# Kernel optimization log

Hardware: AMD Instinct MI355X
Metric: run time of the kernel (lower is better)

Reference implementation:

```python
import jax, jax.numpy as jnp
import numpy as np

N_NODES = 20000  # number of batch nodes (static for segment ops)

def setup_inputs() -> dict:
    key = jax.random.key(0)
    N, E, V, D = N_NODES, 640000, 100000, 64
    ks = jax.random.split(key, 8)
    nodes = jax.random.randint(ks[0], (N,), 0, V)
    neigh_idx = jax.random.randint(ks[1], (E,), 0, V)
    seg_ids = jnp.sort(jax.random.randint(ks[2], (E,), 0, N))  # ragged degrees, sorted by node
    u2e = jax.random.normal(ks[3], (V, D), jnp.float32) * 0.02
    s1 = 1.0 / np.sqrt(2 * D)
    s2 = 1.0 / np.sqrt(D)
    att1_w = jax.random.uniform(ks[4], (2 * D, D), jnp.float32, -s1, s1)
    att1_b = jnp.zeros((D,), jnp.float32)
    att2_w = jax.random.uniform(ks[5], (D, D), jnp.float32, -s2, s2)
    att2_b = jnp.zeros((D,), jnp.float32)
    att3_w = jax.random.uniform(ks[6], (D, 1), jnp.float32, -s2, s2)
    att3_b = jnp.zeros((1,), jnp.float32)
    return dict(nodes=nodes, neigh_idx=neigh_idx, seg_ids=seg_ids, u2e=u2e,
                att1_w=att1_w, att1_b=att1_b, att2_w=att2_w, att2_b=att2_b,
                att3_w=att3_w, att3_b=att3_b)


def reference(nodes, neigh_idx, seg_ids, u2e, att1_w, att1_b, att2_w, att2_b, att3_w, att3_b):
    # Ragged per-node neighbor attention, flattened over all edges.
    e_u = u2e[neigh_idx]              # [E, D] neighbor embeddings
    u_rep = u2e[nodes][seg_ids]       # [E, D] center-node embedding broadcast per edge
    x = jnp.concatenate([e_u, u_rep], axis=1)            # [E, 2D]
    x = jax.nn.relu(x @ att1_w + att1_b)                  # [E, D]
    x = jax.nn.relu(x @ att2_w + att2_b)                  # [E, D]
    logits = (x @ att3_w + att3_b)[:, 0]                  # [E]
    # segment softmax over each node's neighbor set
    m = jax.ops.segment_max(logits, seg_ids, num_segments=N_NODES)
    m = jnp.where(jnp.isfinite(m), m, 0.0)                # guard empty segments
    ex = jnp.exp(logits - m[seg_ids])
    denom = jax.ops.segment_sum(ex, seg_ids, num_segments=N_NODES)
    att = ex / jnp.maximum(denom[seg_ids], 1e-9)          # [E]
    # attention-weighted sum of neighbor embeddings per node (e_u^T @ att_w per node)
    out = jax.ops.segment_sum(att[:, None] * e_u, seg_ids, num_segments=N_NODES)  # [N, D]
    return out
```

## Files before the change

### kernel.cpp

```cpp
#include <hip/hip_runtime.h>
#include <hip/hip_bf16.h>

typedef __attribute__((ext_vector_type(8))) short bf16x8;
typedef __attribute__((ext_vector_type(4))) float f32x4;

__device__ __forceinline__ unsigned short f2bf(float f) {
    unsigned x = __float_as_uint(f);
    unsigned r = (x + 0x7FFF + ((x >> 16) & 1)) >> 16;
    return (unsigned short)r;
}
__device__ __forceinline__ bf16x8 cvt8(const float* __restrict__ p) {
    bf16x8 r;
#pragma unroll
    for (int j = 0; j < 8; ++j) r[j] = (short)f2bf(p[j]);
    return r;
}
__device__ __forceinline__ unsigned pack_relu_bf16(unsigned yv, unsigned zv) {
    float lo = fmaxf(__uint_as_float(yv << 16) + __uint_as_float(zv << 16), 0.0f);
    float hi = fmaxf(__uint_as_float(yv & 0xFFFF0000u) + __uint_as_float(zv & 0xFFFF0000u), 0.0f);
    __hip_bfloat162 p = __float22bfloat162_rn(float2{lo, hi});
    return *(unsigned*)&p;
}

__global__ void prep_bounds_k(const float* __restrict__ w1,
                              const float* __restrict__ w2,
                              const int* __restrict__ segs,
                              unsigned short* __restrict__ w1t,
                              unsigned short* __restrict__ w2t,
                              int* __restrict__ seg_off, int N, int E) {
    int t = threadIdx.x;
    if (blockIdx.x == 0) {
        for (int i = t; i < 128 * 64; i += 256) {
            int k = i >> 6, n = i & 63;
            w1t[n * 128 + k] = f2bf(w1[i]);
        }
        for (int i = t; i < 64 * 64; i += 256) {
            int k = i >> 6, n = i & 63;
            w2t[n * 64 + k] = f2bf(w2[i]);
        }
    } else {
        int idx = (blockIdx.x - 1) * 256 + t;
        if (idx > N) return;
        int l = 0, r = E;
        while (l < r) { int mid = (l + r) >> 1; if (segs[mid] < idx) l = mid + 1; else r = mid; }
        seg_off[idx] = l;
    }
}

template <bool BF>
__launch_bounds__(256)
__global__ void conv_y_z_k(const float* __restrict__ u2e,
                           const int* __restrict__ nodes,
                           const unsigned short* __restrict__ w1t,
                           const float* __restrict__ b1f,
                           unsigned short* __restrict__ u2ebf,
                           unsigned short* __restrict__ Y,
                           unsigned short* __restrict__ z,
                           int V, int N, int yblocks) {
    const int wid = threadIdx.x >> 6;
    const int lane = threadIdx.x & 63;
    const int q = lane >> 4;
    const int m15 = lane & 15;

    if ((int)blockIdx.x < yblocks) {
        const int wbase = (blockIdx.x * 4 + wid) * 16;
        if (wbase >= V) return;
        int row = min(wbase + m15, V - 1);
        const float* p = u2e + (long)row * 64;
        bf16x8 a0 = cvt8(p + q * 8);
        bf16x8 a1 = cvt8(p + 32 + q * 8);
        if (BF && wbase + m15 < V) {
            *(bf16x8*)(u2ebf + (long)row * 64 + q * 8) = a0;
            *(bf16x8*)(u2ebf + (long)row * 64 + 32 + q * 8) = a1;
        }
        f32x4 acc[4];
#pragma unroll
        for (int b = 0; b < 4; ++b) {
            acc[b] = (f32x4){0.f, 0.f, 0.f, 0.f};
            const bf16x8* wrow = (const bf16x8*)(w1t + (b * 16 + m15) * 128);
            acc[b] = __builtin_amdgcn_mfma_f32_16x16x32_bf16(a0, wrow[0 + q], acc[b], 0, 0, 0);
            acc[b] = __builtin_amdgcn_mfma_f32_16x16x32_bf16(a1, wrow[4 + q], acc[b], 0, 0, 0);
        }
#pragma unroll
        for (int b = 0; b < 4; ++b)
#pragma unroll
            for (int r = 0; r < 4; ++r) {
                int rr = wbase + q * 4 + r;
                if (rr < V) Y[(long)rr * 64 + b * 16 + m15] = f2bf(acc[b][r]);
            }
    } else {
        const int wbase = (((int)blockIdx.x - yblocks) * 4 + wid) * 16;
        if (wbase >= N) return;
        int nd = nodes[min(wbase + m15, N - 1)];
        const float* p = u2e + (long)nd * 64;
        bf16x8 a0 = cvt8(p + q * 8);
        bf16x8 a1 = cvt8(p + 32 + q * 8);
        f32x4 acc[4];
#pragma unroll
        for (int b = 0; b < 4; ++b) {
            float bv = b1f[b * 16 + m15];
            acc[b] = (f32x4){bv, bv, bv, bv};
            const bf16x8* wrow = (const bf16x8*)(w1t + (b * 16 + m15) * 128);
            acc[b] = __builtin_amdgcn_mfma_f32_16x16x32_bf16(a0, wrow[8 + q], acc[b], 0, 0, 0);
            acc[b] = __builtin_amdgcn_mfma_f32_16x16x32_bf16(a1, wrow[12 + q], acc[b], 0, 0, 0);
        }
#pragma unroll
        for (int b = 0; b < 4; ++b)
#pragma unroll
            for (int r = 0; r < 4; ++r) {
                int rr = wbase + q * 4 + r;
                if (rr < N) z[(long)rr * 64 + b * 16 + m15] = f2bf(acc[b][r]);
            }
    }
}

__launch_bounds__(256)
__global__ void logits2_k(const int* __restrict__ neigh,
                          const int* __restrict__ segs,
                          const unsigned short* __restrict__ Y,
                          const unsigned short* __restrict__ z,
                          const unsigned short* __restrict__ w2t,
                          const float* __restrict__ b2f,
                          const float* __restrict__ w3f, const float* __restrict__ b3f,
                          float* __restrict__ ex, int E) {
    const int wid = threadIdx.x >> 6;
    const int lane = threadIdx.x & 63;
    const int q = lane >> 4;
    const int m15 = lane & 15;
    const long base = ((long)blockIdx.x * 4 + wid) * 32;
    if (base >= E) return;

    int vi[2], sg[2];
#pragma unroll
    for (int g = 0; g < 2; ++g) {
        long e = base + g * 16 + m15;
        int ec = (int)(e < E ? e : (long)E - 1);
        vi[g] = neigh[ec];
        sg[g] = segs[ec];
    }
    bf16x8 y0[2], y1[2], zz0[2], zz1[2];
#pragma unroll
    for (int g = 0; g < 2; ++g) {
        const unsigned short* yr = Y + (long)vi[g] * 64;
        y0[g] = *(const bf16x8*)(yr + q * 8);
        y1[g] = *(const bf16x8*)(yr + 32 + q * 8);
        const unsigned short* zr = z + (long)sg[g] * 64;
        zz0[g] = *(const bf16x8*)(zr + q * 8);
        zz1[g] = *(const bf16x8*)(zr + 32 + q * 8);
    }

    f32x4 acc[2][4];
#pragma unroll
    for (int g = 0; g < 2; ++g) {
        bf16x8 h0, h1;
#pragma unroll
        for (int j = 0; j < 4; ++j) {
            ((unsigned*)&h0)[j] = pack_relu_bf16(((unsigned*)&y0[g])[j], ((unsigned*)&zz0[g])[j]);
            ((unsigned*)&h1)[j] = pack_relu_bf16(((unsigned*)&y1[g])[j], ((unsigned*)&zz1[g])[j]);
        }
#pragma unroll
        for (int b = 0; b < 4; ++b) {
            float bv = b2f[b * 16 + m15];
            acc[g][b] = (f32x4){bv, bv, bv, bv};
            const bf16x8* wrow = (const bf16x8*)(w2t + (b * 16 + m15) * 64);
            acc[g][b] = __builtin_amdgcn_mfma_f32_16x16x32_bf16(h0, wrow[0 + q], acc[g][b], 0, 0, 0);
            acc[g][b] = __builtin_amdgcn_mfma_f32_16x16x32_bf16(h1, wrow[4 + q], acc[g][b], 0, 0, 0);
        }
    }

    const float b3v = b3f[0];
#pragma unroll
    for (int g = 0; g < 2; ++g)
#pragma unroll
        for (int r = 0; r < 4; ++r) {
            float v = 0.0f;
#pragma unroll
            for (int b = 0; b < 4; ++b) v += fmaxf(acc[g][b][r], 0.0f) * w3f[b * 16 + m15];
            v += __shfl_xor(v, 1);
            v += __shfl_xor(v, 2);
            v += __shfl_xor(v, 4);
            v += __shfl_xor(v, 8);
            long ee = base + g * 16 + q * 4 + r;
            if (m15 == r && ee < E) ex[ee] = __expf(v + b3v);
        }
}

template <bool BF>
__launch_bounds__(256)
__global__ void aggw_k(const int* __restrict__ seg_off,
                       const int* __restrict__ neigh,
                       const unsigned short* __restrict__ u2ebf,
                       const float* __restrict__ u2e,
                       const float* __restrict__ ex,
                       float* __restrict__ out, int N) {
    const int wid = threadIdx.x >> 6;
    const int lane = threadIdx.x & 63;
    const int n = blockIdx.x * 4 + wid;
    if (n >= N) return;
    const int lo = seg_off[n];
    const int hi = seg_off[n + 1];
    const int slot = lane >> 3;
    const int cl = lane & 7;

    float a[8] = {0.f, 0.f, 0.f, 0.f, 0.f, 0.f, 0.f, 0.f};
    float s = 0.0f;

    for (int e = lo + slot; e < hi; e += 8) {
        float w = ex[e];
        int vi = neigh[e];
        s += w;
        if constexpr (BF) {
            bf16x8 v = *(const bf16x8*)(u2ebf + (long)vi * 64 + cl * 8);
            const unsigned* vd = (const unsigned*)&v;
#pragma unroll
            for (int j = 0; j < 4; ++j) {
                a[2 * j]     = fmaf(w, __uint_as_float(vd[j] << 16), a[2 * j]);
                a[2 * j + 1] = fmaf(w, __uint_as_float(vd[j] & 0xFFFF0000u), a[2 * j + 1]);
            }
        } else {
            const float* row = u2e + (long)vi * 64 + cl * 8;
            float4 v0 = *(const float4*)row;
            float4 v1 = *(const float4*)(row + 4);
            a[0] = fmaf(w, v0.x, a[0]); a[1] = fmaf(w, v0.y, a[1]);
            a[2] = fmaf(w, v0.z, a[2]); a[3] = fmaf(w, v0.w, a[3]);
            a[4] = fmaf(w, v1.x, a[4]); a[5] = fmaf(w, v1.y, a[5]);
            a[6] = fmaf(w, v1.z, a[6]); a[7] = fmaf(w, v1.w, a[7]);
        }
    }
#pragma unroll
    for (int msk = 8; msk <= 32; msk <<= 1) {
        s += __shfl_xor(s, msk);
#pragma unroll
        for (int j = 0; j < 8; ++j) a[j] += __shfl_xor(a[j], msk);
    }
    if (slot == 0) {
        float inv = 1.0f / fmaxf(s, 1e-9f);
        float4 o0 = {a[0] * inv, a[1] * inv, a[2] * inv, a[3] * inv};
        float4 o1 = {a[4] * inv, a[5] * inv, a[6] * inv, a[7] * inv};
        float* op = out + (long)n * 64 + cl * 8;
        *(float4*)op = o0;
        *(float4*)(op + 4) = o1;
    }
}

__launch_bounds__(256)
__global__ void logits_fb_k(const int* __restrict__ nodes,
                            const int* __restrict__ neigh,
                            const int* __restrict__ segs,
                            const float* __restrict__ u2e,
                            const unsigned short* __restrict__ w1t,
                            const unsigned short* __restrict__ w2t,
                            const float* __restrict__ b1f, const float* __restrict__ b2f,
                            const float* __restrict__ w3f, const float* __restrict__ b3f,
                            float* __restrict__ ex, int E) {
    __shared__ __align__(16) unsigned short h1buf[4][16 * 72];
    const int wid = threadIdx.x >> 6;
    const int lane = threadIdx.x & 63;
    const int q = lane >> 4;
    const int m15 = lane & 15;
    const long base = ((long)blockIdx.x * 4 + wid) * 16;
    long ee0 = base + m15;
    int e = (int)(ee0 < E ? ee0 : (long)E - 1);
    int ni = neigh[e];
    int ctr = nodes[segs[e]];
    const float* eu = u2e + (long)ni * 64;
    const float* ur = u2e + (long)ctr * 64;
    bf16x8 a0 = cvt8(eu + q * 8), a1 = cvt8(eu + 32 + q * 8);
    bf16x8 a2 = cvt8(ur + q * 8), a3 = cvt8(ur + 32 + q * 8);
    f32x4 acc[4];
#pragma unroll
    for (int b = 0; b < 4; ++b) {
        float bv = b1f[b * 16 + m15];
        acc[b] = (f32x4){bv, bv, bv, bv};
        const bf16x8* wrow = (const bf16x8*)(w1t + (b * 16 + m15) * 128);
        acc[b] = __builtin_amdgcn_mfma_f32_16x16x32_bf16(a0, wrow[0 + q], acc[b], 0, 0, 0);
        acc[b] = __builtin_amdgcn_mfma_f32_16x16x32_bf16(a1, wrow[4 + q], acc[b], 0, 0, 0);
        acc[b] = __builtin_amdgcn_mfma_f32_16x16x32_bf16(a2, wrow[8 + q], acc[b], 0, 0, 0);
        acc[b] = __builtin_amdgcn_mfma_f32_16x16x32_bf16(a3, wrow[12 + q], acc[b], 0, 0, 0);
    }
#pragma unroll
    for (int b = 0; b < 4; ++b)
#pragma unroll
        for (int r = 0; r < 4; ++r)
            h1buf[wid][(q * 4 + r) * 72 + b * 16 + m15] = f2bf(fmaxf(acc[b][r], 0.0f));
    const unsigned short* hrow = &h1buf[wid][m15 * 72];
    bf16x8 h0 = *(const bf16x8*)(hrow + q * 8);
    bf16x8 h1 = *(const bf16x8*)(hrow + 32 + q * 8);
    f32x4 acc2[4];
#pragma unroll
    for (int b = 0; b < 4; ++b) {
        float bv = b2f[b * 16 + m15];
        acc2[b] = (f32x4){bv, bv, bv, bv};
        const bf16x8* wrow = (const bf16x8*)(w2t + (b * 16 + m15) * 64);
        acc2[b] = __builtin_amdgcn_mfma_f32_16x16x32_bf16(h0, wrow[0 + q], acc2[b], 0, 0, 0);
        acc2[b] = __builtin_amdgcn_mfma_f32_16x16x32_bf16(h1, wrow[4 + q], acc2[b], 0, 0, 0);
    }
    float b3v = b3f[0];
#pragma unroll
    for (int r = 0; r < 4; ++r) {
        float v = 0.0f;
#pragma unroll
        for (int b = 0; b < 4; ++b) v += fmaxf(acc2[b][r], 0.0f) * w3f[b * 16 + m15];
        v += __shfl_xor(v, 1);
        v += __shfl_xor(v, 2);
        v += __shfl_xor(v, 4);
        v += __shfl_xor(v, 8);
        long ee = base + q * 4 + r;
        if (m15 == r && ee < E) ex[ee] = __expf(v + b3v);
    }
}

extern "C" void kernel_launch(void* const* d_in, const int* in_sizes, int n_in,
                              void* d_out, int out_size, void* d_ws, size_t ws_size,
                              hipStream_t stream) {
    const int* nodes = (const int*)d_in[0];
    const int* neigh = (const int*)d_in[1];
    const int* segs  = (const int*)d_in[2];
    const float* u2e = (const float*)d_in[3];
    const float* w1  = (const float*)d_in[4];
    const float* b1  = (const float*)d_in[5];
    const float* w2  = (const float*)d_in[6];
    const float* b2  = (const float*)d_in[7];
    const float* w3  = (const float*)d_in[8];
    const float* b3  = (const float*)d_in[9];
    const int N = in_sizes[0];
    const int E = in_sizes[1];
    const long VD = in_sizes[3];
    const int V = (int)(VD / 64);

    char* ws = (char*)d_ws;
    size_t off = 0;
    auto alloc = [&](size_t bytes) { char* p = ws + off; off = (off + bytes + 255) & ~(size_t)255; return p; };
    float* ex = (float*)alloc((size_t)E * 4);
    int* seg_off = (int*)alloc((size_t)(N + 1) * 4);
    unsigned short* w1t = (unsigned short*)alloc(128 * 64 * 2);
    unsigned short* w2t = (unsigned short*)alloc(64 * 64 * 2);
    size_t need_min = off;
    unsigned short* Y = (unsigned short*)alloc((size_t)VD * 2);
    unsigned short* zb = (unsigned short*)alloc((size_t)N * 64 * 2);
    size_t need_t2 = off;
    unsigned short* u2ebf = (unsigned short*)alloc((size_t)VD * 2);
    size_t need_t1 = off;
    (void)need_min;

    float* out = (float*)d_out;

    const int pbblocks = 1 + (N + 256) / 256;
    prep_bounds_k<<<pbblocks, 256, 0, stream>>>(w1, w2, segs, w1t, w2t, seg_off, N, E);

    const int yblocks = ((V + 15) / 16 + 3) / 4;
    const int zblocks = ((N + 15) / 16 + 3) / 4;
    const int lblocks = ((E + 31) / 32 + 3) / 4;
    const int ablocks = (N + 3) / 4;

    if (ws_size >= need_t1) {
        conv_y_z_k<true><<<yblocks + zblocks, 256, 0, stream>>>(
            u2e, nodes, w1t, b1, u2ebf, Y, zb, V, N, yblocks);
        logits2_k<<<lblocks, 256, 0, stream>>>(neigh, segs, Y, zb, w2t, b2, w3, b3, ex, E);
        aggw_k<true><<<ablocks, 256, 0, stream>>>(seg_off, neigh, u2ebf, nullptr, ex, out, N);
    } else if (ws_size >= need_t2) {
        conv_y_z_k<false><<<yblocks + zblocks, 256, 0, stream>>>(
            u2e, nodes, w1t, b1, nullptr, Y, zb, V, N, yblocks);
        logits2_k<<<lblocks, 256, 0, stream>>>(neigh, segs, Y, zb, w2t, b2, w3, b3, ex, E);
        aggw_k<false><<<ablocks, 256, 0, stream>>>(seg_off, neigh, nullptr, u2e, ex, out, N);
    } else {
        const int blocks1 = ((E + 15) / 16 + 3) / 4;
        logits_fb_k<<<blocks1, 256, 0, stream>>>(nodes, neigh, segs, u2e, w1t, w2t,
                                                 b1, b2, w3, b3, ex, E);
        aggw_k<false><<<ablocks, 256, 0, stream>>>(seg_off, neigh, nullptr, u2e, ex, out, N);
    }
}
```

Before: 167.7 us.

## Fuse edge logits and weighted aggregation into one per-node kernel with interleaved rows

After: 182.2 us. 1.09x slower.

```diff
diff --git a/kernel.cpp b/kernel.cpp
--- a/kernel.cpp
+++ b/kernel.cpp
@@ -47,16 +47,14 @@
     }
 }
 
-template <bool BF>
 __launch_bounds__(256)
-__global__ void conv_y_z_k(const float* __restrict__ u2e,
-                           const int* __restrict__ nodes,
-                           const unsigned short* __restrict__ w1t,
-                           const float* __restrict__ b1f,
-                           unsigned short* __restrict__ u2ebf,
-                           unsigned short* __restrict__ Y,
-                           unsigned short* __restrict__ z,
-                           int V, int N, int yblocks) {
+__global__ void conv_yu_z_k(const float* __restrict__ u2e,
+                            const int* __restrict__ nodes,
+                            const unsigned short* __restrict__ w1t,
+                            const float* __restrict__ b1f,
+                            unsigned short* __restrict__ YU,
+                            unsigned short* __restrict__ z,
+                            int V, int N, int yblocks) {
     const int wid = threadIdx.x >> 6;
     const int lane = threadIdx.x & 63;
     const int q = lane >> 4;
@@ -69,9 +67,9 @@
         const float* p = u2e + (long)row * 64;
         bf16x8 a0 = cvt8(p + q * 8);
         bf16x8 a1 = cvt8(p + 32 + q * 8);
-        if (BF && wbase + m15 < V) {
-            *(bf16x8*)(u2ebf + (long)row * 64 + q * 8) = a0;
-            *(bf16x8*)(u2ebf + (long)row * 64 + 32 + q * 8) = a1;
+        if (wbase + m15 < V) {
+            *(bf16x8*)(YU + (long)row * 128 + 64 + q * 8) = a0;
+            *(bf16x8*)(YU + (long)row * 128 + 96 + q * 8) = a1;
         }
         f32x4 acc[4];
 #pragma unroll
@@ -86,7 +84,7 @@
 #pragma unroll
             for (int r = 0; r < 4; ++r) {
                 int rr = wbase + q * 4 + r;
-                if (rr < V) Y[(long)rr * 64 + b * 16 + m15] = f2bf(acc[b][r]);
+                if (rr < V) YU[(long)rr * 128 + b * 16 + m15] = f2bf(acc[b][r]);
             }
     } else {
         const int wbase = (((int)blockIdx.x - yblocks) * 4 + wid) * 16;
@@ -115,131 +113,122 @@
 }
 
 __launch_bounds__(256)
-__global__ void logits2_k(const int* __restrict__ neigh,
-                          const int* __restrict__ segs,
-                          const unsigned short* __restrict__ Y,
-                          const unsigned short* __restrict__ z,
-                          const unsigned short* __restrict__ w2t,
-                          const float* __restrict__ b2f,
-                          const float* __restrict__ w3f, const float* __restrict__ b3f,
-                          float* __restrict__ ex, int E) {
+__global__ void node_k(const int* __restrict__ seg_off,
+                       const int* __restrict__ neigh,
+                       const unsigned short* __restrict__ YU,
+                       const unsigned short* __restrict__ zb,
+                       const unsigned short* __restrict__ w2t,
+                       const float* __restrict__ b2f,
+                       const float* __restrict__ w3f, const float* __restrict__ b3f,
+                       float* __restrict__ out, int N) {
     const int wid = threadIdx.x >> 6;
     const int lane = threadIdx.x & 63;
     const int q = lane >> 4;
     const int m15 = lane & 15;
-    const long base = ((long)blockIdx.x * 4 + wid) * 32;
-    if (base >= E) return;
-
-    int vi[2], sg[2];
-#pragma unroll
-    for (int g = 0; g < 2; ++g) {
-        long e = base + g * 16 + m15;
-        int ec = (int)(e < E ? e : (long)E - 1);
-        vi[g] = neigh[ec];
-        sg[g] = segs[ec];
-    }
-    bf16x8 y0[2], y1[2], zz0[2], zz1[2];
-#pragma unroll
-    for (int g = 0; g < 2; ++g) {
-        const unsigned short* yr = Y + (long)vi[g] * 64;
-        y0[g] = *(const bf16x8*)(yr + q * 8);
-        y1[g] = *(const bf16x8*)(yr + 32 + q * 8);
-        const unsigned short* zr = z + (long)sg[g] * 64;
-        zz0[g] = *(const bf16x8*)(zr + q * 8);
-        zz1[g] = *(const bf16x8*)(zr + 32 + q * 8);
-    }
-
-    f32x4 acc[2][4];
-#pragma unroll
-    for (int g = 0; g < 2; ++g) {
-        bf16x8 h0, h1;
-#pragma unroll
-        for (int j = 0; j < 4; ++j) {
-            ((unsigned*)&h0)[j] = pack_relu_bf16(((unsigned*)&y0[g])[j], ((unsigned*)&zz0[g])[j]);
-            ((unsigned*)&h1)[j] = pack_relu_bf16(((unsigned*)&y1[g])[j], ((unsigned*)&zz1[g])[j]);
-        }
-#pragma unroll
-        for (int b = 0; b < 4; ++b) {
-            float bv = b2f[b * 16 + m15];
-            acc[g][b] = (f32x4){bv, bv, bv, bv};
-            const bf16x8* wrow = (const bf16x8*)(w2t + (b * 16 + m15) * 64);
-            acc[g][b] = __builtin_amdgcn_mfma_f32_16x16x32_bf16(h0, wrow[0 + q], acc[g][b], 0, 0, 0);
-            acc[g][b] = __builtin_amdgcn_mfma_f32_16x16x32_bf16(h1, wrow[4 + q], acc[g][b], 0, 0, 0);
-        }
-    }
-
-    const float b3v = b3f[0];
-#pragma unroll
-    for (int g = 0; g < 2; ++g)
-#pragma unroll
-        for (int r = 0; r < 4; ++r) {
-            float v = 0.0f;
-#pragma unroll
-            for (int b = 0; b < 4; ++b) v += fmaxf(acc[g][b][r], 0.0f) * w3f[b * 16 + m15];
-            v += __shfl_xor(v, 1);
-            v += __shfl_xor(v, 2);
-            v += __shfl_xor(v, 4);
-            v += __shfl_xor(v, 8);
-            long ee = base + g * 16 + q * 4 + r;
-            if (m15 == r && ee < E) ex[ee] = __expf(v + b3v);
-        }
-}
-
-template <bool BF>
-__launch_bounds__(256)
-__global__ void aggw_k(const int* __restrict__ seg_off,
-                       const int* __restrict__ neigh,
-                       const unsigned short* __restrict__ u2ebf,
-                       const float* __restrict__ u2e,
-                       const float* __restrict__ ex,
-                       float* __restrict__ out, int N) {
-    const int wid = threadIdx.x >> 6;
-    const int lane = threadIdx.x & 63;
     const int n = blockIdx.x * 4 + wid;
     if (n >= N) return;
     const int lo = seg_off[n];
     const int hi = seg_off[n + 1];
-    const int slot = lane >> 3;
-    const int cl = lane & 7;
-
-    float a[8] = {0.f, 0.f, 0.f, 0.f, 0.f, 0.f, 0.f, 0.f};
+
+    const unsigned short* zr = zb + (long)n * 64;
+    bf16x8 z0 = *(const bf16x8*)(zr + q * 8);
+    bf16x8 z1 = *(const bf16x8*)(zr + 32 + q * 8);
+
+    bf16x8 wb0[4], wb1[4];
+    float bv[4], w3l[4];
+#pragma unroll
+    for (int b = 0; b < 4; ++b) {
+        const bf16x8* wrow = (const bf16x8*)(w2t + (b * 16 + m15) * 64);
+        wb0[b] = wrow[0 + q];
+        wb1[b] = wrow[4 + q];
+        bv[b] = b2f[b * 16 + m15];
+        w3l[b] = w3f[b * 16 + m15];
+    }
+    const float b3v = b3f[0];
+    const int srcl = ((m15 >> 2) << 4) | m15;
+
+    float a[16];
+#pragma unroll
+    for (int j = 0; j < 16; ++j) a[j] = 0.0f;
     float s = 0.0f;
 
-    for (int e = lo + slot; e < hi; e += 8) {
-        float w = ex[e];
-        int vi = neigh[e];
-        s += w;
-        if constexpr (BF) {
-            bf16x8 v = *(const bf16x8*)(u2ebf + (long)vi * 64 + cl * 8);
-            const unsigned* vd = (const unsigned*)&v;
-#pragma unroll
-            for (int j = 0; j < 4; ++j) {
-                a[2 * j]     = fmaf(w, __uint_as_float(vd[j] << 16), a[2 * j]);
-                a[2 * j + 1] = fmaf(w, __uint_as_float(vd[j] & 0xFFFF0000u), a[2 * j + 1]);
+    for (int cs = lo; cs < hi; cs += 32) {
+#pragma unroll
+        for (int g = 0; g < 2; ++g) {
+            const int gb = cs + g * 16;
+            if (gb < hi) {
+                const int e = gb + m15;
+                const bool val = e < hi;
+                const int ec = val ? e : hi - 1;
+                const int vi = neigh[ec];
+                const unsigned short* row = YU + (long)vi * 128;
+                bf16x8 y0 = *(const bf16x8*)(row + q * 8);
+                bf16x8 y1 = *(const bf16x8*)(row + 32 + q * 8);
+                bf16x8 u0 = *(const bf16x8*)(row + 64 + q * 16);
+                bf16x8 u1 = *(const bf16x8*)(row + 72 + q * 16);
+
+                bf16x8 h0, h1;
+#pragma unroll
+                for (int j = 0; j < 4; ++j) {
+                    ((unsigned*)&h0)[j] = pack_relu_bf16(((unsigned*)&y0)[j], ((unsigned*)&z0)[j]);
+                    ((unsigned*)&h1)[j] = pack_relu_bf16(((unsigned*)&y1)[j], ((unsigned*)&z1)[j]);
+                }
+
+                f32x4 acc[4];
+#pragma unroll
+                for (int b = 0; b < 4; ++b) {
+                    acc[b] = (f32x4){bv[b], bv[b], bv[b], bv[b]};
+                    acc[b] = __builtin_amdgcn_mfma_f32_16x16x32_bf16(h0, wb0[b], acc[b], 0, 0, 0);
+                    acc[b] = __builtin_amdgcn_mfma_f32_16x16x32_bf16(h1, wb1[b], acc[b], 0, 0, 0);
+                }
+
+                float vr[4];
+#pragma unroll
+                for (int r = 0; r < 4; ++r) {
+                    float v = 0.0f;
+#pragma unroll
+                    for (int b = 0; b < 4; ++b) v += fmaxf(acc[b][r], 0.0f) * w3l[b];
+                    v += __shfl_xor(v, 1);
+                    v += __shfl_xor(v, 2);
+                    v += __shfl_xor(v, 4);
+                    v += __shfl_xor(v, 8);
+                    vr[r] = v;
+                }
+                float tmp = (m15 & 2) ? ((m15 & 1) ? vr[3] : vr[2])
+                                      : ((m15 & 1) ? vr[1] : vr[0]);
+                float myv = __shfl(tmp, srcl);
+                float exg = val ? __expf(myv + b3v) : 0.0f;
+                if (q == 0) s += exg;
+
+                const unsigned* ud0 = (const unsigned*)&u0;
+                const unsigned* ud1 = (const unsigned*)&u1;
+#pragma unroll
+                for (int j = 0; j < 4; ++j) {
+                    a[2 * j]      = fmaf(exg, __uint_as_float(ud0[j] << 16), a[2 * j]);
+                    a[2 * j + 1]  = fmaf(exg, __uint_as_float(ud0[j] & 0xFFFF0000u), a[2 * j + 1]);
+                    a[8 + 2 * j]  = fmaf(exg, __uint_as_float(ud1[j] << 16), a[8 + 2 * j]);
+                    a[9 + 2 * j]  = fmaf(exg, __uint_as_float(ud1[j] & 0xFFFF0000u), a[9 + 2 * j]);
+                }
             }
-        } else {
-            const float* row = u2e + (long)vi * 64 + cl * 8;
-            float4 v0 = *(const float4*)row;
-            float4 v1 = *(const float4*)(row + 4);
-            a[0] = fmaf(w, v0.x, a[0]); a[1] = fmaf(w, v0.y, a[1]);
-            a[2] = fmaf(w, v0.z, a[2]); a[3] = fmaf(w, v0.w, a[3]);
-            a[4] = fmaf(w, v1.x, a[4]); a[5] = fmaf(w, v1.y, a[5]);
-            a[6] = fmaf(w, v1.z, a[6]); a[7] = fmaf(w, v1.w, a[7]);
-        }
-    }
-#pragma unroll
-    for (int msk = 8; msk <= 32; msk <<= 1) {
+        }
+    }
+
+#pragma unroll
+    for (int msk = 1; msk <= 8; msk <<= 1) {
         s += __shfl_xor(s, msk);
 #pragma unroll
-        for (int j = 0; j < 8; ++j) a[j] += __shfl_xor(a[j], msk);
-    }
-    if (slot == 0) {
-        float inv = 1.0f / fmaxf(s, 1e-9f);
-        float4 o0 = {a[0] * inv, a[1] * inv, a[2] * inv, a[3] * inv};
-        float4 o1 = {a[4] * inv, a[5] * inv, a[6] * inv, a[7] * inv};
-        float* op = out + (long)n * 64 + cl * 8;
-        *(float4*)op = o0;
-        *(float4*)(op + 4) = o1;
+        for (int j = 0; j < 16; ++j) a[j] += __shfl_xor(a[j], msk);
+    }
+    s = __shfl(s, m15);
+    const float inv = 1.0f / fmaxf(s, 1e-9f);
+    if (m15 == 0) {
+        float* op = out + (long)n * 64 + q * 16;
+#pragma unroll
+        for (int j = 0; j < 4; ++j) {
+            float4 o = {a[4 * j] * inv, a[4 * j + 1] * inv,
+                        a[4 * j + 2] * inv, a[4 * j + 3] * inv};
+            *(float4*)(op + 4 * j) = o;
+        }
     }
 }
 
@@ -270,8 +259,8 @@
     f32x4 acc[4];
 #pragma unroll
     for (int b = 0; b < 4; ++b) {
-        float bv = b1f[b * 16 + m15];
-        acc[b] = (f32x4){bv, bv, bv, bv};
+        float bvv = b1f[b * 16 + m15];
+        acc[b] = (f32x4){bvv, bvv, bvv, bvv};
         const bf16x8* wrow = (const bf16x8*)(w1t + (b * 16 + m15) * 128);
         acc[b] = __builtin_amdgcn_mfma_f32_16x16x32_bf16(a0, wrow[0 + q], acc[b], 0, 0, 0);
         acc[b] = __builtin_amdgcn_mfma_f32_16x16x32_bf16(a1, wrow[4 + q], acc[b], 0, 0, 0);
@@ -289,8 +278,8 @@
     f32x4 acc2[4];
 #pragma unroll
     for (int b = 0; b < 4; ++b) {
-        float bv = b2f[b * 16 + m15];
-        acc2[b] = (f32x4){bv, bv, bv, bv};
+        float bvv = b2f[b * 16 + m15];
+        acc2[b] = (f32x4){bvv, bvv, bvv, bvv};
         const bf16x8* wrow = (const bf16x8*)(w2t + (b * 16 + m15) * 64);
         acc2[b] = __builtin_amdgcn_mfma_f32_16x16x32_bf16(h0, wrow[0 + q], acc2[b], 0, 0, 0);
         acc2[b] = __builtin_amdgcn_mfma_f32_16x16x32_bf16(h1, wrow[4 + q], acc2[b], 0, 0, 0);
@@ -307,6 +296,50 @@
         v += __shfl_xor(v, 8);
         long ee = base + q * 4 + r;
         if (m15 == r && ee < E) ex[ee] = __expf(v + b3v);
+    }
+}
+
+__launch_bounds__(256)
+__global__ void aggw_fb_k(const int* __restrict__ seg_off,
+                          const int* __restrict__ neigh,
+                          const float* __restrict__ u2e,
+                          const float* __restrict__ ex,
+                          float* __restrict__ out, int N) {
+    const int wid = threadIdx.x >> 6;
+    const int lane = threadIdx.x & 63;
+    const int n = blockIdx.x * 4 + wid;
+    if (n >= N) return;
+    const int lo = seg_off[n];
+    const int hi = seg_off[n + 1];
+    const int slot = lane >> 3;
+    const int cl = lane & 7;
+    float a[8] = {0.f, 0.f, 0.f, 0.f, 0.f, 0.f, 0.f, 0.f};
+    float s = 0.0f;
+    for (int e = lo + slot; e < hi; e += 8) {
+        float w = ex[e];
+        int vi = neigh[e];
+        s += w;
+        const float* row = u2e + (long)vi * 64 + cl * 8;
+        float4 v0 = *(const float4*)row;
+        float4 v1 = *(const float4*)(row + 4);
+        a[0] = fmaf(w, v0.x, a[0]); a[1] = fmaf(w, v0.y, a[1]);
+        a[2] = fmaf(w, v0.z, a[2]); a[3] = fmaf(w, v0.w, a[3]);
+        a[4] = fmaf(w, v1.x, a[4]); a[5] = fmaf(w, v1.y, a[5]);
+        a[6] = fmaf(w, v1.z, a[6]); a[7] = fmaf(w, v1.w, a[7]);
+    }
+#pragma unroll
+    for (int msk = 8; msk <= 32; msk <<= 1) {
+        s += __shfl_xor(s, msk);
+#pragma unroll
+        for (int j = 0; j < 8; ++j) a[j] += __shfl_xor(a[j], msk);
+    }
+    if (slot == 0) {
+        float inv = 1.0f / fmaxf(s, 1e-9f);
+        float4 o0 = {a[0] * inv, a[1] * inv, a[2] * inv, a[3] * inv};
+        float4 o1 = {a[4] * inv, a[5] * inv, a[6] * inv, a[7] * inv};
+        float* op = out + (long)n * 64 + cl * 8;
+        *(float4*)op = o0;
+        *(float4*)(op + 4) = o1;
     }
 }
 
@@ -335,13 +368,9 @@
     int* seg_off = (int*)alloc((size_t)(N + 1) * 4);
     unsigned short* w1t = (unsigned short*)alloc(128 * 64 * 2);
     unsigned short* w2t = (unsigned short*)alloc(64 * 64 * 2);
-    size_t need_min = off;
-    unsigned short* Y = (unsigned short*)alloc((size_t)VD * 2);
+    unsigned short* YU = (unsigned short*)alloc((size_t)V * 256);
     unsigned short* zb = (unsigned short*)alloc((size_t)N * 64 * 2);
-    size_t need_t2 = off;
-    unsigned short* u2ebf = (unsigned short*)alloc((size_t)VD * 2);
     size_t need_t1 = off;
-    (void)need_min;
 
     float* out = (float*)d_out;
 
@@ -350,23 +379,17 @@
 
     const int yblocks = ((V + 15) / 16 + 3) / 4;
     const int zblocks = ((N + 15) / 16 + 3) / 4;
-    const int lblocks = ((E + 31) / 32 + 3) / 4;
-    const int ablocks = (N + 3) / 4;
+    const int nblocks = (N + 3) / 4;
 
     if (ws_size >= need_t1) {
-        conv_y_z_k<true><<<yblocks + zblocks, 256, 0, stream>>>(
-            u2e, nodes, w1t, b1, u2ebf, Y, zb, V, N, yblocks);
-        logits2_k<<<lblocks, 256, 0, stream>>>(neigh, segs, Y, zb, w2t, b2, w3, b3, ex, E);
-        aggw_k<true><<<ablocks, 256, 0, stream>>>(seg_off, neigh, u2ebf, nullptr, ex, out, N);
-    } else if (ws_size >= need_t2) {
-        conv_y_z_k<false><<<yblocks + zblocks, 256, 0, stream>>>(
-            u2e, nodes, w1t, b1, nullptr, Y, zb, V, N, yblocks);
-        logits2_k<<<lblocks, 256, 0, stream>>>(neigh, segs, Y, zb, w2t, b2, w3, b3, ex, E);
-        aggw_k<false><<<ablocks, 256, 0, stream>>>(seg_off, neigh, nullptr, u2e, ex, out, N);
+        conv_yu_z_k<<<yblocks + zblocks, 256, 0, stream>>>(
+            u2e, nodes, w1t, b1, YU, zb, V, N, yblocks);
+        node_k<<<nblocks, 256, 0, stream>>>(seg_off, neigh, YU, zb, w2t,
+                                            b2, w3, b3, out, N);
     } else {
         const int blocks1 = ((E + 15) / 16 + 3) / 4;
         logits_fb_k<<<blocks1, 256, 0, stream>>>(nodes, neigh, segs, u2e, w1t, w2t,
                                                  b1, b2, w3, b3, ex, E);
-        aggw_k<false><<<ablocks, 256, 0, stream>>>(seg_off, neigh, nullptr, u2e, ex, out, N);
-    }
-}
+        aggw_fb_k<<<nblocks, 256, 0, stream>>>(seg_off, neigh, u2e, ex, out, N);
+    }
+}
```
